# Optimization experiments

Measured on AMD Instinct MI355X. Metric: run time of the kernel, lower is better.

Reference implementation:

```python
import jax, jax.numpy as jnp
import numpy as np

NUM_EXPERTS = 4
HIDDEN = 768
INTER = 192  # expert_inter; gate_up projects to 2*INTER
TOKENS = 131072


def setup_inputs() -> dict:
    key = jax.random.key(0)
    k1, k2, k3, k4 = jax.random.split(key, 4)
    hidden = jax.random.normal(k1, (TOKENS, HIDDEN), dtype=jnp.float32)
    expert_ids = jax.random.randint(k2, (TOKENS,), 0, NUM_EXPERTS, dtype=jnp.int64)
    gate_up = jax.random.normal(k3, (NUM_EXPERTS, HIDDEN, 2 * INTER), dtype=jnp.float32) * 0.02
    down = jax.random.normal(k4, (NUM_EXPERTS, INTER, HIDDEN), dtype=jnp.float32) * 0.02
    return {"hidden": hidden, "expert_ids": expert_ids, "gate_up": gate_up, "down": down}


def reference(hidden, expert_ids, gate_up, down):
    # Math-equivalent to scatter -> per-expert SwiGLU MLP -> gather back:
    # for each token t with expert e = expert_ids[t]:
    #   out[t] = (silu(x_t @ gate_up[e][:, :F]) * (x_t @ gate_up[e][:, F:])) @ down[e]
    # With E=4 (small), compute per-expert dense and select via one-hot; this is
    # jit-friendly (static shapes) and exactly matches the per-token math.
    E = gate_up.shape[0]
    F = down.shape[1]
    onehot = (expert_ids[None, :] == jnp.arange(E)[:, None]).astype(hidden.dtype)  # [E, T]
    gu = jnp.einsum('th,ehf->etf', hidden, gate_up)      # [E, T, 2F]
    gate, up = gu[..., :F], gu[..., F:]                  # [E, T, F]
    act = jax.nn.silu(gate) * up                         # SwiGLU
    out = jnp.einsum('etf,efh,et->th', act, down, onehot)  # select token's own expert
    return out
```

## Files before the change

kernel.cpp:

```cpp
#include <hip/hip_runtime.h>
#include <hip/hip_bf16.h>

#define NE 4
#define HD 768
#define F2 384
#define F1 192
#define NT 131072
#define TT 128
#define TPE 1024

typedef __attribute__((ext_vector_type(8))) short bf16x8;
typedef __attribute__((ext_vector_type(4))) float f32x4;
typedef __attribute__((ext_vector_type(4))) unsigned int u32x4;

#define LA0 0u
#define LA1 16384u
#define LB0 32768u
#define LB1 81920u
#define LACT 0u
#define LC0 49152u
#define LC1 98304u
#define LTOK 147456u
#define SMEM_BYTES 147968

#define WS_BUCKET_OFF 256
#define WS_GUT_OFF   (WS_BUCKET_OFF + NE*NT*4)
#define WS_DNT_OFF   (WS_GUT_OFF + NE*F2*HD*2)

__device__ __forceinline__ unsigned short f2bf(float x) {
    unsigned int u = __float_as_uint(x);
    return (unsigned short)((u + 0x7fffu + ((u >> 16) & 1u)) >> 16);
}
__device__ __forceinline__ unsigned int pk2(float a, float b) {
    unsigned int ua = __float_as_uint(a), ub = __float_as_uint(b);
    unsigned int lo = (ua + 0x7fffu + ((ua >> 16) & 1u)) >> 16;
    unsigned int hi = (ub + 0x7fffu + ((ub >> 16) & 1u)) & 0xffff0000u;
    return lo | hi;
}

__global__ void route_kernel(const int* __restrict__ ids, int* __restrict__ counts,
                             int* __restrict__ bucket) {
    __shared__ int lc[NE];
    __shared__ int lb[NE];
    int tid = threadIdx.x;
    if (tid < NE) lc[tid] = 0;
    __syncthreads();
    int t = blockIdx.x * blockDim.x + tid;
    int e = ids[t];
    int rank = atomicAdd(&lc[e], 1);
    __syncthreads();
    if (tid < NE) lb[tid] = atomicAdd(&counts[tid], lc[tid]);
    __syncthreads();
    bucket[e * NT + lb[e] + rank] = t;
}

__global__ void convert_kernel(const float* __restrict__ gu, const float* __restrict__ dn,
                               unsigned short* __restrict__ guT, unsigned short* __restrict__ dnT) {
    int idx = blockIdx.x * blockDim.x + threadIdx.x;
    if (idx < NE * F2 * HD) {
        int k = idx % HD; int r = idx / HD; int f = r % F2; int e = r / F2;
        guT[idx] = f2bf(gu[(e * HD + k) * F2 + f]);
    }
    if (idx < NE * HD * F1) {
        int f = idx % F1; int r = idx / F1; int h = r % HD; int e = r / HD;
        dnT[idx] = f2bf(dn[(e * F1 + f) * HD + h]);
    }
}

__global__ __launch_bounds__(512, 1)
void moe_kernel(const float* __restrict__ hidden, const int* __restrict__ counts,
                const int* __restrict__ bucket, const unsigned short* __restrict__ guT,
                const unsigned short* __restrict__ dnT, float* __restrict__ out)
{
    extern __shared__ __align__(16) unsigned char smem[];

    int e = blockIdx.x >> 10;
    int tile = blockIdx.x & (TPE - 1);
    int n_e = counts[e];
    int t0 = tile * TT;
    if (t0 >= n_e) return;

    int tid = threadIdx.x;
    int lane = tid & 63;
    int w = tid >> 6;
    int rw64 = (w >> 2) << 6;
    int w2 = w & 3;
    int lg = lane >> 4;
    int l16 = lane & 15;
    int l7 = l16 & 7;

    int* tokp = (int*)(smem + LTOK);
    if (tid < TT) {
        int idx = t0 + tid; if (idx >= n_e) idx = n_e - 1;
        tokp[tid] = bucket[e * NT + idx];
    }
    __syncthreads();

    int arow = tid >> 2, kq = tid & 3;
    const float* ab = hidden + (size_t)tokp[arow] * HD;
    int colb = tid >> 3, ks = tid & 7;
    const unsigned short* guTe = guT + (size_t)e * F2 * HD;
    const unsigned short* dnTe = dnT + (size_t)e * HD * F1;

    unsigned awb0 = (unsigned)(arow * 128 + ((kq ^ (arow & 7)) << 4));
    unsigned awb1 = (unsigned)(arow * 128 + (((4 + kq) ^ (arow & 7)) << 4));
    unsigned bwb  = (unsigned)(colb * 128 + ((ks ^ (colb & 7)) << 4));

    f32x4 av0, av1, av2, av3;
    bf16x8 bv[6];

    auto issueA = [&](int k0) {
        const float* p = ab + k0 + kq * 8;
        av0 = *(const f32x4*)p;          av1 = *(const f32x4*)(p + 4);
        av2 = *(const f32x4*)(p + 32);   av3 = *(const f32x4*)(p + 36);
    };
    auto writeA = [&](unsigned base) {
        u32x4 lo = {pk2(av0.x,av0.y), pk2(av0.z,av0.w), pk2(av1.x,av1.y), pk2(av1.z,av1.w)};
        u32x4 hi = {pk2(av2.x,av2.y), pk2(av2.z,av2.w), pk2(av3.x,av3.y), pk2(av3.z,av3.w)};
        *(u32x4*)(smem + base + awb0) = lo;
        *(u32x4*)(smem + base + awb1) = hi;
    };
    auto issueB = [&](int k0) {
        #pragma unroll
        for (int jj = 0; jj < 6; ++jj)
            bv[jj] = *(const bf16x8*)(guTe + (size_t)(colb + jj * 64) * HD + k0 + ks * 8);
    };
    auto issueB2 = [&](int half, int s) {
        #pragma unroll
        for (int jj = 0; jj < 6; ++jj)
            bv[jj] = *(const bf16x8*)(dnTe + (size_t)(half * F2 + colb + jj * 64) * F1 + s * 64 + ks * 8);
    };
    auto writeB = [&](unsigned base) {
        #pragma unroll
        for (int jj = 0; jj < 6; ++jj)
            *(bf16x8*)(smem + base + bwb + jj * 8192u) = bv[jj];
    };

    unsigned arb[4], brb1[6], b2rb[6], a2rb[4];
    #pragma unroll
    for (int mt = 0; mt < 4; ++mt) {
        arb[mt] = (unsigned)((rw64 + mt * 16 + l16) * 128);
        a2rb[mt] = (unsigned)(LACT + (rw64 + mt * 16 + l16) * 384);
    }
    #pragma unroll
    for (int nt = 0; nt < 6; ++nt) {
        int col = w2 * 48 + (nt < 3 ? nt * 16 : 192 + (nt - 3) * 16) + l16;
        brb1[nt] = (unsigned)(col * 128);
        b2rb[nt] = (unsigned)((w2 * 96 + nt * 16 + l16) * 128);
    }
    unsigned xk0 = (unsigned)((lg ^ l7) << 4);
    unsigned xk1 = (unsigned)(((4 + lg) ^ l7) << 4);

    const f32x4 fzero = {0.f, 0.f, 0.f, 0.f};
    f32x4 acc[4][6];
    #pragma unroll
    for (int mt = 0; mt < 4; ++mt)
        #pragma unroll
        for (int nt = 0; nt < 6; ++nt) acc[mt][nt] = fzero;

    issueA(0); issueB(0);
    writeA(LA0); writeB(LB0);
    __syncthreads();

    #pragma unroll 1
    for (int t = 0; t < 12; ++t) {
        unsigned Ab  = (t & 1) ? LA1 : LA0;
        unsigned Bb  = (t & 1) ? LB1 : LB0;
        unsigned Abn = (t & 1) ? LA0 : LA1;
        unsigned Bbn = (t & 1) ? LB0 : LB1;
        if (t < 11) { issueA((t + 1) * 64); issueB((t + 1) * 64); }

        bf16x8 Af[2][4], Bf[2][6];
        #pragma unroll
        for (int mt = 0; mt < 4; ++mt) {
            Af[0][mt] = *(const bf16x8*)(smem + Ab + arb[mt] + xk0);
            Af[1][mt] = *(const bf16x8*)(smem + Ab + arb[mt] + xk1);
        }
        #pragma unroll
        for (int nt = 0; nt < 6; ++nt) {
            Bf[0][nt] = *(const bf16x8*)(smem + Bb + brb1[nt] + xk0);
            Bf[1][nt] = *(const bf16x8*)(smem + Bb + brb1[nt] + xk1);
        }
        #pragma unroll
        for (int kk = 0; kk < 2; ++kk)
            #pragma unroll
            for (int nt = 0; nt < 6; ++nt)
                #pragma unroll
                for (int mt = 0; mt < 4; ++mt)
                    acc[mt][nt] = __builtin_amdgcn_mfma_f32_16x16x32_bf16(Af[kk][mt], Bf[kk][nt], acc[mt][nt], 0, 0, 0);

        if (t < 11) { writeA(Abn); writeB(Bbn); }
        __syncthreads();
    }

    issueB2(0, 0);
    #pragma unroll
    for (int mt = 0; mt < 4; ++mt)
        #pragma unroll
        for (int nt = 0; nt < 3; ++nt)
            #pragma unroll
            for (int p = 0; p < 4; ++p) {
                float g = acc[mt][nt][p];
                float u = acc[mt][nt + 3][p];
                float s = g / (1.f + __expf(-g));
                int row = rw64 + mt * 16 + 4 * lg + p;
                int f = w2 * 48 + nt * 16 + l16;
                unsigned b = (unsigned)(LACT + row * 384 + (((f >> 3) ^ (row & 7)) << 4) + (f & 7) * 2);
                *(unsigned short*)(smem + b) = f2bf(s * u);
            }
    writeB(LC0);
    __syncthreads();

    int strow[4][4];
    #pragma unroll
    for (int mt = 0; mt < 4; ++mt)
        #pragma unroll
        for (int p = 0; p < 4; ++p)
            strow[mt][p] = tokp[rw64 + mt * 16 + 4 * lg + p];

    #pragma unroll 1
    for (int half = 0; half < 2; ++half) {
        f32x4 c2[4][6];
        #pragma unroll
        for (int mt = 0; mt < 4; ++mt)
            #pragma unroll
            for (int nt = 0; nt < 6; ++nt) c2[mt][nt] = fzero;

        #pragma unroll
        for (int s = 0; s < 3; ++s) {
            unsigned Cb  = ((half + s) & 1) ? LC1 : LC0;
            unsigned Cbn = ((half + s) & 1) ? LC0 : LC1;
            int do_next = (s < 2) || (half == 0);
            if (s < 2) issueB2(half, s + 1);
            else if (half == 0) issueB2(1, 0);

            bf16x8 A2[2][4], B2f[2][6];
            #pragma unroll
            for (int mt = 0; mt < 4; ++mt) {
                A2[0][mt] = *(const bf16x8*)(smem + a2rb[mt] + s * 128 + xk0);
                A2[1][mt] = *(const bf16x8*)(smem + a2rb[mt] + s * 128 + xk1);
            }
            #pragma unroll
            for (int nt = 0; nt < 6; ++nt) {
                B2f[0][nt] = *(const bf16x8*)(smem + Cb + b2rb[nt] + xk0);
                B2f[1][nt] = *(const bf16x8*)(smem + Cb + b2rb[nt] + xk1);
            }
            #pragma unroll
            for (int kk = 0; kk < 2; ++kk)
                #pragma unroll
                for (int nt = 0; nt < 6; ++nt)
                    #pragma unroll
                    for (int mt = 0; mt < 4; ++mt)
                        c2[mt][nt] = __builtin_amdgcn_mfma_f32_16x16x32_bf16(A2[kk][mt], B2f[kk][nt], c2[mt][nt], 0, 0, 0);

            if (do_next) {
                writeB(Cbn);
                __syncthreads();
            }
        }

        #pragma unroll
        for (int mt = 0; mt < 4; ++mt)
            #pragma unroll
            for (int p = 0; p < 4; ++p) {
                int rl = rw64 + mt * 16 + 4 * lg + p;
                if (t0 + rl < n_e) {
                    float* orow = out + (size_t)strow[mt][p] * HD + half * F2 + w2 * 96 + l16;
                    #pragma unroll
                    for (int nt = 0; nt < 6; ++nt)
                        orow[nt * 16] = c2[mt][nt][p];
                }
            }
    }
}

extern "C" void kernel_launch(void* const* d_in, const int* in_sizes, int n_in,
                              void* d_out, int out_size, void* d_ws, size_t ws_size,
                              hipStream_t stream) {
    (void)in_sizes; (void)n_in; (void)out_size; (void)ws_size;
    const float* hidden = (const float*)d_in[0];
    const int*   ids    = (const int*)d_in[1];
    const float* gu     = (const float*)d_in[2];
    const float* dn     = (const float*)d_in[3];
    float* out = (float*)d_out;

    char* ws = (char*)d_ws;
    int* counts = (int*)ws;
    int* bucket = (int*)(ws + WS_BUCKET_OFF);
    unsigned short* guT = (unsigned short*)(ws + WS_GUT_OFF);
    unsigned short* dnT = (unsigned short*)(ws + WS_DNT_OFF);

    hipMemsetAsync(d_ws, 0, 64, stream);
    route_kernel<<<NT / 256, 256, 0, stream>>>(ids, counts, bucket);
    convert_kernel<<<(NE * F2 * HD + 255) / 256, 256, 0, stream>>>(gu, dn, guT, dnT);
    moe_kernel<<<NE * TPE, 512, SMEM_BYTES, stream>>>(hidden, counts, bucket, guT, dnT, out);
}
```

Baseline: 297.3 us.

## Split fused MoE kernel into two GEMM kernels with bf16 activation buffer

Splits the fused gate_up/SwiGLU/down kernel into two kernels. The first writes bf16 SwiGLU activations to a workspace buffer. The second reads them back for the down projection. Both use 256-token tiles with the output columns split across blocks for more parallelism, and load weights and activations with global_load_lds direct-to-LDS copies. The cost is an extra activation round-trip through global memory. The fused kernel stays as a fallback when the workspace is too small, and its LDS swizzle is also changed.

```diff
diff --git a/kernel.cpp b/kernel.cpp
--- a/kernel.cpp
+++ b/kernel.cpp
@@ -6,26 +6,16 @@
 #define F2 384
 #define F1 192
 #define NT 131072
-#define TT 128
-#define TPE 1024
 
 typedef __attribute__((ext_vector_type(8))) short bf16x8;
 typedef __attribute__((ext_vector_type(4))) float f32x4;
 typedef __attribute__((ext_vector_type(4))) unsigned int u32x4;
 
-#define LA0 0u
-#define LA1 16384u
-#define LB0 32768u
-#define LB1 81920u
-#define LACT 0u
-#define LC0 49152u
-#define LC1 98304u
-#define LTOK 147456u
-#define SMEM_BYTES 147968
-
 #define WS_BUCKET_OFF 256
 #define WS_GUT_OFF   (WS_BUCKET_OFF + NE*NT*4)
 #define WS_DNT_OFF   (WS_GUT_OFF + NE*F2*HD*2)
+#define WS_ACT_OFF   (WS_DNT_OFF + NE*F1*HD*2)
+#define WS_NEED      ((size_t)WS_ACT_OFF + (size_t)NT*F1*2)
 
 __device__ __forceinline__ unsigned short f2bf(float x) {
     unsigned int u = __float_as_uint(x);
@@ -37,6 +27,9 @@
     unsigned int hi = (ub + 0x7fffu + ((ub >> 16) & 1u)) & 0xffff0000u;
     return lo | hi;
 }
+#define GLL(srcp, ldsoff) \
+    __builtin_amdgcn_global_load_lds((const __attribute__((address_space(1))) void*)(srcp), \
+        (__attribute__((address_space(3))) void*)(smem + (ldsoff)), 16, 0, 0)
 
 __global__ void route_kernel(const int* __restrict__ ids, int* __restrict__ counts,
                              int* __restrict__ bucket) {
@@ -67,17 +60,266 @@
     }
 }
 
+#define G1_LA0 0u
+#define G1_LA1 32768u
+#define G1_LB0 65536u
+#define G1_LB1 90112u
+#define G_SMEM 114688
+
 __global__ __launch_bounds__(512, 1)
-void moe_kernel(const float* __restrict__ hidden, const int* __restrict__ counts,
-                const int* __restrict__ bucket, const unsigned short* __restrict__ guT,
-                const unsigned short* __restrict__ dnT, float* __restrict__ out)
+void gemm1_kernel(const float* __restrict__ hidden, const int* __restrict__ counts,
+                  const int* __restrict__ bucket, const unsigned short* __restrict__ guT,
+                  unsigned short* __restrict__ act)
 {
     extern __shared__ __align__(16) unsigned char smem[];
-
+    int bid = blockIdx.x;
+    int e = bid >> 10;
+    int rem = bid & 1023;
+    int tile = rem >> 1, s = rem & 1;
+    int n_e = counts[e];
+    int t0 = tile * 256;
+    if (t0 >= n_e) return;
+
+    int tid = threadIdx.x, lane = tid & 63, w = tid >> 6;
+    int rq = w >> 1, ch = w & 1;
+    int lg = lane >> 4, l16 = lane & 15;
+    const int* bkt = bucket + e * NT;
+
+    int arow = tid >> 1, kh = tid & 1;
+    int ai = t0 + arow; if (ai >= n_e) ai = n_e - 1;
+    const float* aptr = hidden + (size_t)bkt[ai] * HD + kh * 32;
+    unsigned awb[4];
+    #pragma unroll
+    for (int j = 0; j < 4; ++j)
+        awb[j] = (unsigned)(arow * 128 + (((kh * 4 + j) ^ (arow & 7)) << 4));
+
+    const unsigned short* guTe = guT + (size_t)e * F2 * HD;
+    const unsigned short* bsrc[3];
+    unsigned bdst[3];
+    #pragma unroll
+    for (int i = 0; i < 3; ++i) {
+        int c = w * 24 + i * 8 + (lane >> 3);
+        int kc = lane & 7;
+        int gcol = (c < 96) ? (s * 96 + c) : (192 + s * 96 + (c - 96));
+        bsrc[i] = guTe + (size_t)gcol * HD + ((kc ^ (c & 7)) * 8);
+        bdst[i] = (unsigned)(w * 3072 + i * 1024);
+    }
+
+    unsigned arb[4], brb[6];
+    #pragma unroll
+    for (int mt = 0; mt < 4; ++mt) arb[mt] = (unsigned)((rq * 64 + mt * 16 + l16) * 128);
+    #pragma unroll
+    for (int nt = 0; nt < 6; ++nt) {
+        int tc = ch * 48 + (nt < 3 ? nt * 16 : 96 + (nt - 3) * 16) + l16;
+        brb[nt] = (unsigned)(tc * 128);
+    }
+    unsigned xs0 = (unsigned)((lg ^ (l16 & 7)) << 4);
+    unsigned xs1 = (unsigned)(((4 + lg) ^ (l16 & 7)) << 4);
+
+    f32x4 av[8];
+    auto issueA = [&](int k0) {
+        const f32x4* p = (const f32x4*)(aptr + k0);
+        #pragma unroll
+        for (int j = 0; j < 8; ++j) av[j] = p[j];
+    };
+    auto writeA = [&](unsigned base) {
+        #pragma unroll
+        for (int j = 0; j < 4; ++j) {
+            u32x4 v = { pk2(av[2*j].x, av[2*j].y), pk2(av[2*j].z, av[2*j].w),
+                        pk2(av[2*j+1].x, av[2*j+1].y), pk2(av[2*j+1].z, av[2*j+1].w) };
+            *(u32x4*)(smem + base + awb[j]) = v;
+        }
+    };
+    auto gloadB = [&](unsigned base, int k0) {
+        #pragma unroll
+        for (int i = 0; i < 3; ++i) GLL(bsrc[i] + k0, base + bdst[i]);
+    };
+
+    const f32x4 fzero = {0.f, 0.f, 0.f, 0.f};
+    f32x4 acc[4][6];
+    #pragma unroll
+    for (int mt = 0; mt < 4; ++mt)
+        #pragma unroll
+        for (int nt = 0; nt < 6; ++nt) acc[mt][nt] = fzero;
+
+    issueA(0); gloadB(G1_LB0, 0); writeA(G1_LA0);
+    __syncthreads();
+
+    #pragma unroll 1
+    for (int t = 0; t < 12; ++t) {
+        unsigned Ab  = (t & 1) ? G1_LA1 : G1_LA0;
+        unsigned Bb  = (t & 1) ? G1_LB1 : G1_LB0;
+        unsigned Abn = (t & 1) ? G1_LA0 : G1_LA1;
+        unsigned Bbn = (t & 1) ? G1_LB0 : G1_LB1;
+        if (t < 11) { gloadB(Bbn, (t + 1) * 64); issueA((t + 1) * 64); }
+
+        #pragma unroll
+        for (int kk = 0; kk < 2; ++kk) {
+            unsigned xs = kk ? xs1 : xs0;
+            bf16x8 Af[4], Bf[6];
+            #pragma unroll
+            for (int mt = 0; mt < 4; ++mt) Af[mt] = *(const bf16x8*)(smem + Ab + arb[mt] + xs);
+            #pragma unroll
+            for (int nt = 0; nt < 6; ++nt) Bf[nt] = *(const bf16x8*)(smem + Bb + brb[nt] + xs);
+            #pragma unroll
+            for (int nt = 0; nt < 6; ++nt)
+                #pragma unroll
+                for (int mt = 0; mt < 4; ++mt)
+                    acc[mt][nt] = __builtin_amdgcn_mfma_f32_16x16x32_bf16(Af[mt], Bf[nt], acc[mt][nt], 0, 0, 0);
+        }
+
+        if (t < 11) writeA(Abn);
+        __syncthreads();
+    }
+
+    #pragma unroll
+    for (int mt = 0; mt < 4; ++mt) {
+        #pragma unroll
+        for (int p = 0; p < 4; ++p) {
+            int r = rq * 64 + mt * 16 + 4 * lg + p;
+            int idx = t0 + r;
+            if (idx < n_e) {
+                unsigned short* arow_p = act + (size_t)bkt[idx] * F1 + s * 96 + ch * 48 + l16;
+                #pragma unroll
+                for (int nt = 0; nt < 3; ++nt) {
+                    float g = acc[mt][nt][p];
+                    float u = acc[mt][nt + 3][p];
+                    float sv = g / (1.f + __expf(-g));
+                    arow_p[nt * 16] = f2bf(sv * u);
+                }
+            }
+        }
+    }
+}
+
+__global__ __launch_bounds__(512, 1)
+void gemm2_kernel(const int* __restrict__ counts, const int* __restrict__ bucket,
+                  const unsigned short* __restrict__ dnT, const unsigned short* __restrict__ act,
+                  float* __restrict__ out)
+{
+    extern __shared__ __align__(16) unsigned char smem[];
+    int bid = blockIdx.x;
+    int e = bid >> 11;
+    int rem = bid & 2047;
+    int tile = rem >> 2, sl = rem & 3;
+    int n_e = counts[e];
+    int t0 = tile * 256;
+    if (t0 >= n_e) return;
+
+    int tid = threadIdx.x, lane = tid & 63, w = tid >> 6;
+    int rq = w >> 1, ch = w & 1;
+    int lg = lane >> 4, l16 = lane & 15;
+    const int* bkt = bucket + e * NT;
+    const unsigned short* dnTe = dnT + (size_t)e * HD * F1;
+
+    const unsigned short* asrc[4];
+    unsigned adst[4];
+    #pragma unroll
+    for (int i = 0; i < 4; ++i) {
+        int r = w * 32 + i * 8 + (lane >> 3);
+        int kc = lane & 7;
+        int ri = t0 + r; if (ri >= n_e) ri = n_e - 1;
+        asrc[i] = act + (size_t)bkt[ri] * F1 + ((kc ^ (r & 7)) * 8);
+        adst[i] = (unsigned)(w * 4096 + i * 1024);
+    }
+    const unsigned short* bsrc[3];
+    unsigned bdst[3];
+    #pragma unroll
+    for (int i = 0; i < 3; ++i) {
+        int c = w * 24 + i * 8 + (lane >> 3);
+        int kc = lane & 7;
+        bsrc[i] = dnTe + (size_t)(sl * 192 + c) * F1 + ((kc ^ (c & 7)) * 8);
+        bdst[i] = (unsigned)(w * 3072 + i * 1024);
+    }
+
+    unsigned arb[4], brb[6];
+    #pragma unroll
+    for (int mt = 0; mt < 4; ++mt) arb[mt] = (unsigned)((rq * 64 + mt * 16 + l16) * 128);
+    #pragma unroll
+    for (int nt = 0; nt < 6; ++nt) brb[nt] = (unsigned)((ch * 96 + nt * 16 + l16) * 128);
+    unsigned xs0 = (unsigned)((lg ^ (l16 & 7)) << 4);
+    unsigned xs1 = (unsigned)(((4 + lg) ^ (l16 & 7)) << 4);
+
+    auto gload = [&](unsigned Ab, unsigned Bb, int k0) {
+        #pragma unroll
+        for (int i = 0; i < 4; ++i) GLL(asrc[i] + k0, Ab + adst[i]);
+        #pragma unroll
+        for (int i = 0; i < 3; ++i) GLL(bsrc[i] + k0, Bb + bdst[i]);
+    };
+
+    const f32x4 fzero = {0.f, 0.f, 0.f, 0.f};
+    f32x4 acc[4][6];
+    #pragma unroll
+    for (int mt = 0; mt < 4; ++mt)
+        #pragma unroll
+        for (int nt = 0; nt < 6; ++nt) acc[mt][nt] = fzero;
+
+    gload(G1_LA0, G1_LB0, 0);
+    __syncthreads();
+
+    #pragma unroll 1
+    for (int t = 0; t < 3; ++t) {
+        unsigned Ab  = (t & 1) ? G1_LA1 : G1_LA0;
+        unsigned Bb  = (t & 1) ? G1_LB1 : G1_LB0;
+        unsigned Abn = (t & 1) ? G1_LA0 : G1_LA1;
+        unsigned Bbn = (t & 1) ? G1_LB0 : G1_LB1;
+        if (t < 2) gload(Abn, Bbn, (t + 1) * 64);
+
+        #pragma unroll
+        for (int kk = 0; kk < 2; ++kk) {
+            unsigned xs = kk ? xs1 : xs0;
+            bf16x8 Af[4], Bf[6];
+            #pragma unroll
+            for (int mt = 0; mt < 4; ++mt) Af[mt] = *(const bf16x8*)(smem + Ab + arb[mt] + xs);
+            #pragma unroll
+            for (int nt = 0; nt < 6; ++nt) Bf[nt] = *(const bf16x8*)(smem + Bb + brb[nt] + xs);
+            #pragma unroll
+            for (int nt = 0; nt < 6; ++nt)
+                #pragma unroll
+                for (int mt = 0; mt < 4; ++mt)
+                    acc[mt][nt] = __builtin_amdgcn_mfma_f32_16x16x32_bf16(Af[mt], Bf[nt], acc[mt][nt], 0, 0, 0);
+        }
+        if (t < 2) __syncthreads();
+    }
+
+    #pragma unroll
+    for (int mt = 0; mt < 4; ++mt) {
+        #pragma unroll
+        for (int p = 0; p < 4; ++p) {
+            int r = rq * 64 + mt * 16 + 4 * lg + p;
+            int idx = t0 + r;
+            if (idx < n_e) {
+                float* orow = out + (size_t)bkt[idx] * HD + sl * 192 + ch * 96 + l16;
+                #pragma unroll
+                for (int nt = 0; nt < 6; ++nt)
+                    orow[nt * 16] = acc[mt][nt][p];
+            }
+        }
+    }
+}
+
+#define FTT 128
+#define FTPE 1024
+#define F_LA0 0u
+#define F_LA1 16384u
+#define F_LB0 32768u
+#define F_LB1 81920u
+#define F_LACT 0u
+#define F_LC0 49152u
+#define F_LC1 98304u
+#define F_LTOK 147456u
+#define F_SMEM 147968
+
+__global__ __launch_bounds__(512, 1)
+void moe_fused_kernel(const float* __restrict__ hidden, const int* __restrict__ counts,
+                      const int* __restrict__ bucket, const unsigned short* __restrict__ guT,
+                      const unsigned short* __restrict__ dnT, float* __restrict__ out)
+{
+    extern __shared__ __align__(16) unsigned char smem[];
     int e = blockIdx.x >> 10;
-    int tile = blockIdx.x & (TPE - 1);
+    int tile = blockIdx.x & (FTPE - 1);
     int n_e = counts[e];
-    int t0 = tile * TT;
+    int t0 = tile * FTT;
     if (t0 >= n_e) return;
 
     int tid = threadIdx.x;
@@ -87,10 +329,9 @@
     int w2 = w & 3;
     int lg = lane >> 4;
     int l16 = lane & 15;
-    int l7 = l16 & 7;
-
-    int* tokp = (int*)(smem + LTOK);
-    if (tid < TT) {
+
+    int* tokp = (int*)(smem + F_LTOK);
+    if (tid < FTT) {
         int idx = t0 + tid; if (idx >= n_e) idx = n_e - 1;
         tokp[tid] = bucket[e * NT + idx];
     }
@@ -125,10 +366,10 @@
         for (int jj = 0; jj < 6; ++jj)
             bv[jj] = *(const bf16x8*)(guTe + (size_t)(colb + jj * 64) * HD + k0 + ks * 8);
     };
-    auto issueB2 = [&](int half, int s) {
+    auto issueB2 = [&](int half, int sx) {
         #pragma unroll
         for (int jj = 0; jj < 6; ++jj)
-            bv[jj] = *(const bf16x8*)(dnTe + (size_t)(half * F2 + colb + jj * 64) * F1 + s * 64 + ks * 8);
+            bv[jj] = *(const bf16x8*)(dnTe + (size_t)(half * F2 + colb + jj * 64) * F1 + sx * 64 + ks * 8);
     };
     auto writeB = [&](unsigned base) {
         #pragma unroll
@@ -140,7 +381,7 @@
     #pragma unroll
     for (int mt = 0; mt < 4; ++mt) {
         arb[mt] = (unsigned)((rw64 + mt * 16 + l16) * 128);
-        a2rb[mt] = (unsigned)(LACT + (rw64 + mt * 16 + l16) * 384);
+        a2rb[mt] = (unsigned)(F_LACT + (rw64 + mt * 16 + l16) * 384);
     }
     #pragma unroll
     for (int nt = 0; nt < 6; ++nt) {
@@ -148,8 +389,8 @@
         brb1[nt] = (unsigned)(col * 128);
         b2rb[nt] = (unsigned)((w2 * 96 + nt * 16 + l16) * 128);
     }
-    unsigned xk0 = (unsigned)((lg ^ l7) << 4);
-    unsigned xk1 = (unsigned)(((4 + lg) ^ l7) << 4);
+    unsigned xk0 = (unsigned)((lg ^ (l16 & 7)) << 4);
+    unsigned xk1 = (unsigned)(((4 + lg) ^ (l16 & 7)) << 4);
 
     const f32x4 fzero = {0.f, 0.f, 0.f, 0.f};
     f32x4 acc[4][6];
@@ -159,15 +400,15 @@
         for (int nt = 0; nt < 6; ++nt) acc[mt][nt] = fzero;
 
     issueA(0); issueB(0);
-    writeA(LA0); writeB(LB0);
+    writeA(F_LA0); writeB(F_LB0);
     __syncthreads();
 
     #pragma unroll 1
     for (int t = 0; t < 12; ++t) {
-        unsigned Ab  = (t & 1) ? LA1 : LA0;
-        unsigned Bb  = (t & 1) ? LB1 : LB0;
-        unsigned Abn = (t & 1) ? LA0 : LA1;
-        unsigned Bbn = (t & 1) ? LB0 : LB1;
+        unsigned Ab  = (t & 1) ? F_LA1 : F_LA0;
+        unsigned Bb  = (t & 1) ? F_LB1 : F_LB0;
+        unsigned Abn = (t & 1) ? F_LA0 : F_LA1;
+        unsigned Bbn = (t & 1) ? F_LB0 : F_LB1;
         if (t < 11) { issueA((t + 1) * 64); issueB((t + 1) * 64); }
 
         bf16x8 Af[2][4], Bf[2][6];
@@ -202,13 +443,14 @@
             for (int p = 0; p < 4; ++p) {
                 float g = acc[mt][nt][p];
                 float u = acc[mt][nt + 3][p];
-                float s = g / (1.f + __expf(-g));
+                float sv = g / (1.f + __expf(-g));
                 int row = rw64 + mt * 16 + 4 * lg + p;
                 int f = w2 * 48 + nt * 16 + l16;
-                unsigned b = (unsigned)(LACT + row * 384 + (((f >> 3) ^ (row & 7)) << 4) + (f & 7) * 2);
-                *(unsigned short*)(smem + b) = f2bf(s * u);
-            }
-    writeB(LC0);
+                int c = f >> 3;
+                unsigned b = (unsigned)(F_LACT + row * 384 + (((c & 24) | ((c & 7) ^ (row & 7))) << 4) + (f & 7) * 2);
+                *(unsigned short*)(smem + b) = f2bf(sv * u);
+            }
+    writeB(F_LC0);
     __syncthreads();
 
     int strow[4][4];
@@ -227,18 +469,19 @@
             for (int nt = 0; nt < 6; ++nt) c2[mt][nt] = fzero;
 
         #pragma unroll
-        for (int s = 0; s < 3; ++s) {
-            unsigned Cb  = ((half + s) & 1) ? LC1 : LC0;
-            unsigned Cbn = ((half + s) & 1) ? LC0 : LC1;
-            int do_next = (s < 2) || (half == 0);
-            if (s < 2) issueB2(half, s + 1);
+        for (int sx = 0; sx < 3; ++sx) {
+            unsigned Cb  = ((half + sx) & 1) ? F_LC1 : F_LC0;
+            unsigned Cbn = ((half + sx) & 1) ? F_LC0 : F_LC1;
+            int do_next = (sx < 2) || (half == 0);
+            if (sx < 2) issueB2(half, sx + 1);
             else if (half == 0) issueB2(1, 0);
 
             bf16x8 A2[2][4], B2f[2][6];
             #pragma unroll
             for (int mt = 0; mt < 4; ++mt) {
-                A2[0][mt] = *(const bf16x8*)(smem + a2rb[mt] + s * 128 + xk0);
-                A2[1][mt] = *(const bf16x8*)(smem + a2rb[mt] + s * 128 + xk1);
+                int c0 = sx * 4;
+                A2[0][mt] = *(const bf16x8*)(smem + a2rb[mt] + ((((c0 + lg) & 24) | (((c0 + lg) & 7) ^ (l16 & 7))) << 4));
+                A2[1][mt] = *(const bf16x8*)(smem + a2rb[mt] + ((((c0 + 4 + lg) & 24) | (((c0 + 4 + lg) & 7) ^ (l16 & 7))) << 4));
             }
             #pragma unroll
             for (int nt = 0; nt < 6; ++nt) {
@@ -277,7 +520,7 @@
 extern "C" void kernel_launch(void* const* d_in, const int* in_sizes, int n_in,
                               void* d_out, int out_size, void* d_ws, size_t ws_size,
                               hipStream_t stream) {
-    (void)in_sizes; (void)n_in; (void)out_size; (void)ws_size;
+    (void)in_sizes; (void)n_in; (void)out_size;
     const float* hidden = (const float*)d_in[0];
     const int*   ids    = (const int*)d_in[1];
     const float* gu     = (const float*)d_in[2];
@@ -293,5 +536,12 @@
     hipMemsetAsync(d_ws, 0, 64, stream);
     route_kernel<<<NT / 256, 256, 0, stream>>>(ids, counts, bucket);
     convert_kernel<<<(NE * F2 * HD + 255) / 256, 256, 0, stream>>>(gu, dn, guT, dnT);
-    moe_kernel<<<NE * TPE, 512, SMEM_BYTES, stream>>>(hidden, counts, bucket, guT, dnT, out);
-}
+
+    if (ws_size >= WS_NEED) {
+        unsigned short* act = (unsigned short*)(ws + WS_ACT_OFF);
+        gemm1_kernel<<<NE * 1024, 512, G_SMEM, stream>>>(hidden, counts, bucket, guT, act);
+        gemm2_kernel<<<NE * 2048, 512, G_SMEM, stream>>>(counts, bucket, dnT, act, out);
+    } else {
+        moe_fused_kernel<<<NE * FTPE, 512, F_SMEM, stream>>>(hidden, counts, bucket, guT, dnT, out);
+    }
+}
```

Result: slower. 423.4 us (+42.4%).
